# Optimization experiments

Hardware: AMD Instinct MI355X
Metric: run time of the kernel (lower is better)

## Reference

```python
import jax, jax.numpy as jnp
import numpy as np

BG_W = 1.0
DILATED_BG_W = 5.0
EDGE_W = 20.0
KSIZE = 3


def setup_inputs() -> dict:
    key = jax.random.key(0)
    k1, k2 = jax.random.split(key)
    B, C, H, W = 16, 1, 1024, 1024
    pred = jax.random.normal(k1, (B, C, H, W), dtype=jnp.float32)
    target = (jax.random.uniform(k2, (B, C, H, W)) < 0.05).astype(jnp.float32)
    return {"pred": pred, "target": target}


def _dilate(target):
    # cv2.dilate with KSIZExKSIZE rect kernel == max pool, stride 1, SAME padding
    return jax.lax.reduce_window(
        target, -jnp.inf, jax.lax.max,
        window_dimensions=(1, 1, KSIZE, KSIZE),
        window_strides=(1, 1, 1, 1),
        padding="SAME",
    )


def reference(pred, target):
    dilated = _dilate(target)
    # weight: edge pixels (target>0.5) -> EDGE_W, else dilated band -> DILATED_BG_W, else BG_W
    weight = jnp.where(target > 0.5, EDGE_W,
                       jnp.where(dilated > 0.5, DILATED_BG_W, BG_W))
    # binary_cross_entropy_with_logits, reduction='none', then mean
    x = pred
    losses = weight * (jnp.maximum(x, 0.0) - x * target + jnp.log1p(jnp.exp(-jnp.abs(x))))
    return jnp.mean(losses)
```

## Files before the change

kernel.cpp:

```cpp
#include <hip/hip_runtime.h>

#define HH 1024
#define WW 1024
#define BAND 8
#define NT 256

__device__ __forceinline__ float fmax3(float a, float b, float c) {
    return fmaxf(a, fmaxf(b, c));
}

__device__ __forceinline__ float loss_elem(float x, float t, float dil) {
    float w = fmaf(15.0f, t, fmaf(4.0f, dil, 1.0f));
    float a  = fabsf(x);
    float sp = __logf(1.0f + __expf(-a));
    return w * (fmaxf(x, 0.0f) - x * t + sp);
}

template <bool PER_WAVE>
__global__ __launch_bounds__(NT, 4) void dilatedweightBCE_main(
        const float* __restrict__ pred,
        const float* __restrict__ target,
        float* __restrict__ partial) {
    __shared__ float swave[NT / 64];

    const int t    = threadIdx.x;
    const int lane = t & 63;
    const int wv   = t >> 6;
    const int c    = t * 4;

    const int l    = blockIdx.x;
    const int xcd  = l & 7;
    const int j    = l >> 3;
    const int img  = j >> 4;
    const int band = j & 15;
    const int h0   = (xcd * 16 + band) * BAND;

    const float* timg = target + (size_t)img * HH * WW;
    const float* pimg = pred   + (size_t)img * HH * WW;
    const float4 zero = make_float4(0.0f, 0.0f, 0.0f, 0.0f);

    float4 tr[BAND + 2];
    tr[0] = (h0 > 0) ? *(const float4*)(timg + (size_t)(h0 - 1) * WW + c) : zero;
    #pragma unroll
    for (int r = 0; r < BAND; ++r)
        tr[r + 1] = *(const float4*)(timg + (size_t)(h0 + r) * WW + c);
    tr[BAND + 1] = (h0 + BAND < HH)
                 ? *(const float4*)(timg + (size_t)(h0 + BAND) * WW + c) : zero;

    float4 xr[BAND];
    #pragma unroll
    for (int r = 0; r < BAND; ++r)
        xr[r] = *(const float4*)(pimg + (size_t)(h0 + r) * WW + c);

    float halo[BAND];
    #pragma unroll
    for (int r = 0; r < BAND; ++r) halo[r] = 0.0f;
    if (lane == 0 || lane == 63) {
        const int pc = (lane == 0) ? c - 1 : c + 4;
        if (pc >= 0 && pc < WW) {
            float hv[BAND + 2];
            hv[0] = (h0 > 0) ? timg[(size_t)(h0 - 1) * WW + pc] : 0.0f;
            #pragma unroll
            for (int r = 0; r < BAND; ++r)
                hv[r + 1] = timg[(size_t)(h0 + r) * WW + pc];
            hv[BAND + 1] = (h0 + BAND < HH)
                         ? timg[(size_t)(h0 + BAND) * WW + pc] : 0.0f;
            #pragma unroll
            for (int r = 0; r < BAND; ++r)
                halo[r] = fmax3(hv[r], hv[r + 1], hv[r + 2]);
        }
    }

    float s = 0.0f;
    #pragma unroll
    for (int r = 0; r < BAND; ++r) {
        float4 a = tr[r], m = tr[r + 1], d = tr[r + 2];
        float4 vm = make_float4(fmax3(a.x, m.x, d.x), fmax3(a.y, m.y, d.y),
                                fmax3(a.z, m.z, d.z), fmax3(a.w, m.w, d.w));

        float lft = __shfl_up(vm.w, 1);
        float rgt = __shfl_down(vm.x, 1);
        if (lane == 0)  lft = halo[r];
        if (lane == 63) rgt = halo[r];

        float d0 = fmax3(lft,  vm.x, vm.y);
        float d1 = fmax3(vm.x, vm.y, vm.z);
        float d2 = fmax3(vm.y, vm.z, vm.w);
        float d3 = fmax3(vm.z, vm.w, rgt);

        float4 x = xr[r];
        s += loss_elem(x.x, m.x, d0);
        s += loss_elem(x.y, m.y, d1);
        s += loss_elem(x.z, m.z, d2);
        s += loss_elem(x.w, m.w, d3);
    }

    #pragma unroll
    for (int off = 32; off > 0; off >>= 1)
        s += __shfl_down(s, off);

    if (PER_WAVE) {
        if (lane == 0)
            partial[(size_t)l * (NT / 64) + wv] = s;
    } else {
        if (lane == 0) swave[wv] = s;
        __syncthreads();
        if (t == 0) {
            float tot = 0.0f;
            #pragma unroll
            for (int i = 0; i < NT / 64; ++i) tot += swave[i];
            partial[l] = tot;
        }
    }
}

__global__ __launch_bounds__(1024) void dilatedweightBCE_reduce(
        const float* __restrict__ partial,
        float* __restrict__ out,
        int npart4,
        float inv_n) {
    __shared__ float swave[16];
    const int t = threadIdx.x;

    float s = 0.0f;
    const float4* p4 = (const float4*)partial;
    for (int i = t; i < npart4; i += 1024) {
        float4 v = p4[i];
        s += v.x + v.y + v.z + v.w;
    }

    #pragma unroll
    for (int off = 32; off > 0; off >>= 1)
        s += __shfl_down(s, off);

    const int lane = t & 63;
    if (lane == 0) swave[t >> 6] = s;
    __syncthreads();
    if (t == 0) {
        float tot = 0.0f;
        #pragma unroll
        for (int i = 0; i < 16; ++i) tot += swave[i];
        out[0] = tot * inv_n;
    }
}

extern "C" void kernel_launch(void* const* d_in, const int* in_sizes, int n_in,
                              void* d_out, int out_size, void* d_ws, size_t ws_size,
                              hipStream_t stream) {
    const float* pred   = (const float*)d_in[0];
    const float* target = (const float*)d_in[1];
    float* out     = (float*)d_out;
    float* partial = (float*)d_ws;

    const int n  = in_sizes[0];
    const int Bn = n / (HH * WW);
    const int nblocks = (HH / BAND) * Bn;

    const size_t need = (size_t)nblocks * (NT / 64) * sizeof(float);
    if (ws_size >= need) {
        dilatedweightBCE_main<true><<<nblocks, NT, 0, stream>>>(pred, target, partial);
        dilatedweightBCE_reduce<<<1, 1024, 0, stream>>>(partial, out,
                                                        nblocks * (NT / 64) / 4,
                                                        1.0f / (float)n);
    } else {
        dilatedweightBCE_main<false><<<nblocks, NT, 0, stream>>>(pred, target, partial);
        dilatedweightBCE_reduce<<<1, 1024, 0, stream>>>(partial, out,
                                                        nblocks / 4,
                                                        1.0f / (float)n);
    }
}
```

Baseline: 141.9 us.

## Stage band tiles in LDS via direct global-to-LDS loads with 1024-thread blocks

```diff
diff --git a/kernel.cpp b/kernel.cpp
--- a/kernel.cpp
+++ b/kernel.cpp
@@ -3,7 +3,10 @@
 #define HH 1024
 #define WW 1024
 #define BAND 8
-#define NT 256
+#define NT 1024
+#define TROWS (BAND + 2)
+#define LDS_T (TROWS * WW)
+#define LDS_P (BAND * WW)
 
 __device__ __forceinline__ float fmax3(float a, float b, float c) {
     return fmaxf(a, fmaxf(b, c));
@@ -16,17 +19,24 @@
     return w * (fmaxf(x, 0.0f) - x * t + sp);
 }
 
+__device__ __forceinline__ void dma16(const float* g, float* l) {
+    __builtin_amdgcn_global_load_lds(
+        (const __attribute__((address_space(1))) void*)g,
+        (__attribute__((address_space(3))) void*)l,
+        16, 0, 0);
+}
+
 template <bool PER_WAVE>
-__global__ __launch_bounds__(NT, 4) void dilatedweightBCE_main(
+__global__ __launch_bounds__(NT) void dilatedweightBCE_main(
         const float* __restrict__ pred,
         const float* __restrict__ target,
         float* __restrict__ partial) {
-    __shared__ float swave[NT / 64];
+    __shared__ float ldsT[LDS_T];
+    __shared__ float ldsP[LDS_P];
 
     const int t    = threadIdx.x;
     const int lane = t & 63;
     const int wv   = t >> 6;
-    const int c    = t * 4;
 
     const int l    = blockIdx.x;
     const int xcd  = l & 7;
@@ -37,58 +47,74 @@
 
     const float* timg = target + (size_t)img * HH * WW;
     const float* pimg = pred   + (size_t)img * HH * WW;
-    const float4 zero = make_float4(0.0f, 0.0f, 0.0f, 0.0f);
 
-    float4 tr[BAND + 2];
-    tr[0] = (h0 > 0) ? *(const float4*)(timg + (size_t)(h0 - 1) * WW + c) : zero;
-    #pragma unroll
-    for (int r = 0; r < BAND; ++r)
-        tr[r + 1] = *(const float4*)(timg + (size_t)(h0 + r) * WW + c);
-    tr[BAND + 1] = (h0 + BAND < HH)
-                 ? *(const float4*)(timg + (size_t)(h0 + BAND) * WW + c) : zero;
+    const float4 zero4 = make_float4(0.0f, 0.0f, 0.0f, 0.0f);
+    if (h0 == 0 && t < 256) ((float4*)ldsT)[t] = zero4;
+    if (h0 + BAND == HH && t >= 256 && t < 512)
+        ((float4*)ldsT)[2048 + t] = zero4;
 
-    float4 xr[BAND];
-    #pragma unroll
-    for (int r = 0; r < BAND; ++r)
-        xr[r] = *(const float4*)(pimg + (size_t)(h0 + r) * WW + c);
+    const float* srcT = timg + (long long)(h0 - 1) * WW;
+    {
+        if (!(h0 == 0 && t < 256))
+            dma16(srcT + (size_t)t * 4, ldsT + (size_t)t * 4);
+        dma16(srcT + (size_t)(1024 + t) * 4, ldsT + (size_t)(1024 + t) * 4);
+        if (t < 512 && !(h0 + BAND == HH && t >= 256))
+            dma16(srcT + (size_t)(2048 + t) * 4, ldsT + (size_t)(2048 + t) * 4);
+    }
+    {
+        const float* srcP = pimg + (size_t)h0 * WW;
+        dma16(srcP + (size_t)t * 4,          ldsP + (size_t)t * 4);
+        dma16(srcP + (size_t)(1024 + t) * 4, ldsP + (size_t)(1024 + t) * 4);
+    }
 
-    float halo[BAND];
-    #pragma unroll
-    for (int r = 0; r < BAND; ++r) halo[r] = 0.0f;
+    __syncthreads();
+
+    const int strip = t & 255;
+    const int c     = strip * 4;
+    const int rp    = t >> 8;
+    const int o0    = rp * 2;
+
+    float4 T0 = *(const float4*)(ldsT + (o0    ) * WW + c);
+    float4 T1 = *(const float4*)(ldsT + (o0 + 1) * WW + c);
+    float4 T2 = *(const float4*)(ldsT + (o0 + 2) * WW + c);
+    float4 T3 = *(const float4*)(ldsT + (o0 + 3) * WW + c);
+    float4 X0 = *(const float4*)(ldsP + (o0    ) * WW + c);
+    float4 X1 = *(const float4*)(ldsP + (o0 + 1) * WW + c);
+
+    float hl[2] = {0.0f, 0.0f};
     if (lane == 0 || lane == 63) {
         const int pc = (lane == 0) ? c - 1 : c + 4;
         if (pc >= 0 && pc < WW) {
-            float hv[BAND + 2];
-            hv[0] = (h0 > 0) ? timg[(size_t)(h0 - 1) * WW + pc] : 0.0f;
-            #pragma unroll
-            for (int r = 0; r < BAND; ++r)
-                hv[r + 1] = timg[(size_t)(h0 + r) * WW + pc];
-            hv[BAND + 1] = (h0 + BAND < HH)
-                         ? timg[(size_t)(h0 + BAND) * WW + pc] : 0.0f;
-            #pragma unroll
-            for (int r = 0; r < BAND; ++r)
-                halo[r] = fmax3(hv[r], hv[r + 1], hv[r + 2]);
+            float h0v = ldsT[(o0    ) * WW + pc];
+            float h1v = ldsT[(o0 + 1) * WW + pc];
+            float h2v = ldsT[(o0 + 2) * WW + pc];
+            float h3v = ldsT[(o0 + 3) * WW + pc];
+            hl[0] = fmax3(h0v, h1v, h2v);
+            hl[1] = fmax3(h1v, h2v, h3v);
         }
     }
 
     float s = 0.0f;
     #pragma unroll
-    for (int r = 0; r < BAND; ++r) {
-        float4 a = tr[r], m = tr[r + 1], d = tr[r + 2];
+    for (int k = 0; k < 2; ++k) {
+        float4 a = (k == 0) ? T0 : T1;
+        float4 m = (k == 0) ? T1 : T2;
+        float4 d = (k == 0) ? T2 : T3;
+        float4 x = (k == 0) ? X0 : X1;
+
         float4 vm = make_float4(fmax3(a.x, m.x, d.x), fmax3(a.y, m.y, d.y),
                                 fmax3(a.z, m.z, d.z), fmax3(a.w, m.w, d.w));
 
         float lft = __shfl_up(vm.w, 1);
         float rgt = __shfl_down(vm.x, 1);
-        if (lane == 0)  lft = halo[r];
-        if (lane == 63) rgt = halo[r];
+        if (lane == 0)  lft = hl[k];
+        if (lane == 63) rgt = hl[k];
 
         float d0 = fmax3(lft,  vm.x, vm.y);
         float d1 = fmax3(vm.x, vm.y, vm.z);
         float d2 = fmax3(vm.y, vm.z, vm.w);
         float d3 = fmax3(vm.z, vm.w, rgt);
 
-        float4 x = xr[r];
         s += loss_elem(x.x, m.x, d0);
         s += loss_elem(x.y, m.y, d1);
         s += loss_elem(x.z, m.z, d2);
@@ -100,15 +126,15 @@
         s += __shfl_down(s, off);
 
     if (PER_WAVE) {
-        if (lane == 0)
-            partial[(size_t)l * (NT / 64) + wv] = s;
+        if (lane == 0) partial[(size_t)l * 16 + wv] = s;
     } else {
-        if (lane == 0) swave[wv] = s;
+        __syncthreads();
+        if (lane == 0) ldsT[wv] = s;
         __syncthreads();
         if (t == 0) {
             float tot = 0.0f;
             #pragma unroll
-            for (int i = 0; i < NT / 64; ++i) tot += swave[i];
+            for (int i = 0; i < 16; ++i) tot += ldsT[i];
             partial[l] = tot;
         }
     }
@@ -156,11 +182,11 @@
     const int Bn = n / (HH * WW);
     const int nblocks = (HH / BAND) * Bn;
 
-    const size_t need = (size_t)nblocks * (NT / 64) * sizeof(float);
+    const size_t need = (size_t)nblocks * 16 * sizeof(float);
     if (ws_size >= need) {
         dilatedweightBCE_main<true><<<nblocks, NT, 0, stream>>>(pred, target, partial);
         dilatedweightBCE_reduce<<<1, 1024, 0, stream>>>(partial, out,
-                                                        nblocks * (NT / 64) / 4,
+                                                        nblocks * 16 / 4,
                                                         1.0f / (float)n);
     } else {
         dilatedweightBCE_main<false><<<nblocks, NT, 0, stream>>>(pred, target, partial);
```

Result: no change. 144.3 us (+1.7%).
